# Kernel optimization log

Measured on AMD Instinct MI355X. Metric: run time of the kernel, lower is better.

Reference implementation:

```python
import jax, jax.numpy as jnp
import numpy as np

D = 64      # n_embd (== head_size in this module)
H = 8       # n_heads
B = 4
T = 2048    # seq len == block_size
EPS = 1e-5


def layernorm(x, g, b):
    mu = jnp.mean(x, axis=-1, keepdims=True)
    var = jnp.mean(jnp.square(x - mu), axis=-1, keepdims=True)
    return (x - mu) * jax.lax.rsqrt(var + EPS) * g + b


def setup_inputs() -> dict:
    key = jax.random.key(0)
    ks = jax.random.split(key, 16)
    s = 1.0 / np.sqrt(D)
    inp = {
        'inputs': jax.random.normal(ks[0], (B, T, D), jnp.float32),
        # per-head QKV linears: weight [H, D, D] (in, out), bias [H, D]
        'Wq': jax.random.uniform(ks[1], (H, D, D), jnp.float32, -s, s),
        'bq': jax.random.uniform(ks[2], (H, D), jnp.float32, -s, s),
        'Wk': jax.random.uniform(ks[3], (H, D, D), jnp.float32, -s, s),
        'bk': jax.random.uniform(ks[4], (H, D), jnp.float32, -s, s),
        'Wv': jax.random.uniform(ks[5], (H, D, D), jnp.float32, -s, s),
        'bv': jax.random.uniform(ks[6], (H, D), jnp.float32, -s, s),
        # projection: Linear(H*D -> D)
        'Wp': jax.random.uniform(ks[7], (H * D, D), jnp.float32, -1/np.sqrt(H*D), 1/np.sqrt(H*D)),
        'bp': jax.random.uniform(ks[8], (D,), jnp.float32, -1/np.sqrt(H*D), 1/np.sqrt(H*D)),
        # FFN: D -> 4D -> D
        'W1': jax.random.uniform(ks[9], (D, 4 * D), jnp.float32, -s, s),
        'b1': jax.random.uniform(ks[10], (4 * D,), jnp.float32, -s, s),
        'W2': jax.random.uniform(ks[11], (4 * D, D), jnp.float32, -1/np.sqrt(4*D), 1/np.sqrt(4*D)),
        'b2': jax.random.uniform(ks[12], (D,), jnp.float32, -1/np.sqrt(4*D), 1/np.sqrt(4*D)),
        'g1': jnp.ones((D,), jnp.float32), 'be1': jnp.zeros((D,), jnp.float32),
        'g2': jnp.ones((D,), jnp.float32), 'be2': jnp.zeros((D,), jnp.float32),
    }
    return inp


def reference(inputs, Wq, bq, Wk, bk, Wv, bv, Wp, bp, W1, b1, W2, b2, g1, be1, g2, be2):
    x = inputs
    # per-head full-width QKV: [H, B, T, D]
    q = jnp.einsum('btd,hde->hbte', x, Wq) + bq[:, None, None, :]
    k = jnp.einsum('btd,hde->hbte', x, Wk) + bk[:, None, None, :]
    v = jnp.einsum('btd,hde->hbte', x, Wv) + bv[:, None, None, :]
    # unscaled scores (module has no 1/sqrt(d) scaling)
    scores = jnp.einsum('hbte,hbse->hbts', q, k)  # [H, B, T, T]
    causal = jnp.tril(jnp.ones((T, T), bool))
    scores = jnp.where(causal, scores, -jnp.inf)
    attn = jax.nn.softmax(scores, axis=-1)
    out = jnp.einsum('hbts,hbse->hbte', attn, v)  # [H, B, T, D]
    # torch.cat over heads along last dim -> [B, T, H*D]
    cat = jnp.transpose(out, (1, 2, 0, 3)).reshape(B, T, H * D)
    attn_out = cat @ Wp + bp
    h1 = layernorm(x + attn_out, g1, be1)
    ffn = jax.nn.relu(h1 @ W1 + b1) @ W2 + b2
    return layernorm(h1 + ffn, g2, be2)
```

## Files before the change

kernel.cpp:

```cpp
#include <hip/hip_runtime.h>
#include <hip/hip_bf16.h>
#include <stdint.h>

#define Dd 64
#define Hh 8
#define Bb 4
#define Tt 2048
#define NT (Bb * Tt)

typedef __attribute__((ext_vector_type(4))) float f32x4;
typedef __attribute__((ext_vector_type(8))) __bf16 bf16x8;
typedef __attribute__((ext_vector_type(8))) uint16_t u16x8;
typedef __attribute__((ext_vector_type(4))) uint16_t u16x4;

__device__ __forceinline__ uint16_t f2bf_fast(float f) {
    union { __bf16 h; uint16_t u; } c; c.h = (__bf16)f; return c.u;
}
__device__ __forceinline__ uint32_t pkbf(float a, float b) {
    return (uint32_t)f2bf_fast(a) | ((uint32_t)f2bf_fast(b) << 16);
}

#define SWZ(row, k)   ((row) * 72  + ((k) ^ ((((row) >> 3) & 7) << 3)))
#define PSZ(q, k)     ((q)  * 72  + ((k) ^ ((((q)  >> 2) & 3) << 3)))
#define HSZ(q, k)     ((q)  * 264 + ((k) ^ ((((q)  >> 2) & 3) << 3)))
#define W2SWZ(col, k) ((col) * 264 + ((k) ^ ((((col) >> 3) & 7) << 3)))
#define WPSWZ(col, k) ((col) * 520 + ((k) ^ ((((col) >> 3) & 7) << 3)))

__global__ __launch_bounds__(256) void setup_kernel(
    const float* __restrict__ Wp, const float* __restrict__ W1,
    const float* __restrict__ W2,
    uint16_t* __restrict__ WptS, uint16_t* __restrict__ W1g,
    uint16_t* __restrict__ W2g)
{
    const int bid = blockIdx.x, t = threadIdx.x;
    if (bid < 8) {
        const int j = bid;
#pragma unroll
        for (int p = 0; p < 16; ++p) {
            int idx = p * 256 + t;
            int col = idx & 63, k = j * 64 + (idx >> 6);
            WptS[WPSWZ(col, k)] = f2bf_fast(Wp[(size_t)k * 64 + col]);
        }
    } else if (bid < 12) {
        const int j = bid - 8;
#pragma unroll
        for (int p = 0; p < 16; ++p) {
            int e = j * 4096 + p * 256 + t;
            int col = e & 255, k = e >> 8;
            W1g[SWZ(col, k)] = f2bf_fast(W1[(size_t)k * 256 + col]);
        }
    } else {
        const int j = bid - 12;
#pragma unroll
        for (int p = 0; p < 16; ++p) {
            int e = j * 4096 + p * 256 + t;
            int col = e & 63, k = e >> 6;
            W2g[W2SWZ(col, k)] = f2bf_fast(W2[(size_t)k * 64 + col]);
        }
    }
}

__global__ __launch_bounds__(256) void qkv_kernel(
    const float* __restrict__ x,
    const float* __restrict__ Wq, const float* __restrict__ bq,
    const float* __restrict__ Wk, const float* __restrict__ bk,
    const float* __restrict__ Wv, const float* __restrict__ bv,
    uint16_t* __restrict__ qb, uint16_t* __restrict__ kb, uint16_t* __restrict__ vb)
{
    __shared__ uint16_t WtF[64 * 72];
    const int rt = blockIdx.x, h = blockIdx.y, m = blockIdx.z;
    const float* W    = (m == 0) ? Wq : (m == 1) ? Wk : Wv;
    const float* bias = (m == 0) ? bq : (m == 1) ? bk : bv;
    uint16_t*    out  = (m == 0) ? qb : (m == 1) ? kb : vb;
    const int t = threadIdx.x, lane = t & 63, w = t >> 6;
    const int l15 = lane & 15, g = lane >> 4;

#pragma unroll
    for (int p = 0; p < 4; ++p) {
        int idx = p * 256 + t;
        int r = idx >> 4, c4 = (idx & 15) * 4;
        f32x4 wv = *(const f32x4*)&W[(size_t)(h * 64 + r) * 64 + c4];
#pragma unroll
        for (int j = 0; j < 4; ++j) WtF[SWZ(c4 + j, r)] = f2bf_fast(wv[j]);
    }
    const int row = rt * 64 + w * 16 + l15;
    union { u16x8 u; bf16x8 b; } a0, a1;
    {
        f32x4 x0 = *(const f32x4*)&x[(size_t)row * 64 + g * 8];
        f32x4 x1 = *(const f32x4*)&x[(size_t)row * 64 + g * 8 + 4];
        f32x4 x2 = *(const f32x4*)&x[(size_t)row * 64 + 32 + g * 8];
        f32x4 x3 = *(const f32x4*)&x[(size_t)row * 64 + 32 + g * 8 + 4];
#pragma unroll
        for (int j = 0; j < 4; ++j) {
            a0.u[j] = f2bf_fast(x0[j]); a0.u[4 + j] = f2bf_fast(x1[j]);
            a1.u[j] = f2bf_fast(x2[j]); a1.u[4 + j] = f2bf_fast(x3[j]);
        }
    }
    __syncthreads();

    f32x4 acc[4] = {};
#pragma unroll
    for (int ct = 0; ct < 4; ++ct) {
        bf16x8 b0 = *(const bf16x8*)&WtF[SWZ(ct * 16 + l15, g * 8)];
        bf16x8 b1 = *(const bf16x8*)&WtF[SWZ(ct * 16 + l15, 32 + g * 8)];
        acc[ct] = __builtin_amdgcn_mfma_f32_16x16x32_bf16(a0.b, b0, acc[ct], 0, 0, 0);
        acc[ct] = __builtin_amdgcn_mfma_f32_16x16x32_bf16(a1.b, b1, acc[ct], 0, 0, 0);
    }
#pragma unroll
    for (int ct = 0; ct < 4; ++ct) {
        float bb = bias[h * 64 + ct * 16 + l15];
#pragma unroll
        for (int rr = 0; rr < 4; ++rr) {
            int orow = rt * 64 + w * 16 + g * 4 + rr;
            out[((size_t)h * NT + orow) * 64 + ct * 16 + l15] =
                f2bf_fast(acc[ct][rr] + bb);
        }
    }
}

__global__ __launch_bounds__(128) void attn_kernel5(
    const uint16_t* __restrict__ qb, const uint16_t* __restrict__ kb,
    const uint16_t* __restrict__ vb, uint16_t* __restrict__ cat)
{
    __shared__ uint16_t KsF[2][64 * 72];
    __shared__ uint16_t VtF[2][64 * 72];
    const int bid = blockIdx.x;
    const int lbid = (bid & 7) * 128 + (bid >> 3);
    const int pairid = lbid & 31;
    const int hb = lbid >> 5;
    const int h = hb & 7, b = hb >> 3;
    const int t = threadIdx.x, lane = t & 63, w = t >> 6;
    const int l15 = lane & 15, g = lane >> 4;
    const size_t base = ((size_t)h * NT + (size_t)b * Tt) * 64;
    const uint16_t* Qh = qb + base;
    const uint16_t* Kh = kb + base;
    const uint16_t* Vh = vb + base;

    for (int ph = 0; ph < 2; ++ph) {
        const int qt32 = ph ? (63 - pairid) : pairid;
        bf16x8 aq0, aq1;
        {
            int qrow = qt32 * 32 + w * 16 + l15;
            aq0 = *(const bf16x8*)&Qh[(size_t)qrow * 64 + g * 8];
            aq1 = *(const bf16x8*)&Qh[(size_t)qrow * 64 + 32 + g * 8];
        }
        f32x4 o[4] = {};
        float m_run = -INFINITY, l_run = 0.f;

        __syncthreads();
#pragma unroll
        for (int i = 0; i < 4; ++i) {
            int slot = i * 128 + t;
            int r = slot >> 3, c8 = (slot & 7) * 8;
            u16x8 kk = *(const u16x8*)&Kh[(size_t)r * 64 + c8];
            u16x8 vv = *(const u16x8*)&Vh[(size_t)r * 64 + c8];
            *(u16x8*)&KsF[0][SWZ(r, c8)] = kk;
#pragma unroll
            for (int j = 0; j < 8; ++j) VtF[0][SWZ(c8 + j, r)] = vv[j];
        }
        __syncthreads();

        const int nkv = (qt32 >> 1) + 1;
        for (int kv = 0; kv < nkv; ++kv) {
            const int cur = kv & 1;
            const bool pf = (kv + 1) < nkv;
            u16x8 pK[4], pV[4];
            if (pf) {
#pragma unroll
                for (int i = 0; i < 4; ++i) {
                    int slot = i * 128 + t;
                    int r = (kv + 1) * 64 + (slot >> 3), c8 = (slot & 7) * 8;
                    pK[i] = *(const u16x8*)&Kh[(size_t)r * 64 + c8];
                    pV[i] = *(const u16x8*)&Vh[(size_t)r * 64 + c8];
                }
            }
            f32x4 s[4];
#pragma unroll
            for (int kt = 0; kt < 4; ++kt) {
                bf16x8 bk0 = *(const bf16x8*)&KsF[cur][SWZ(kt * 16 + l15, g * 8)];
                bf16x8 bk1 = *(const bf16x8*)&KsF[cur][SWZ(kt * 16 + l15, 32 + g * 8)];
                f32x4 z = {};
                z = __builtin_amdgcn_mfma_f32_16x16x32_bf16(bk0, aq0, z, 0, 0, 0);
                z = __builtin_amdgcn_mfma_f32_16x16x32_bf16(bk1, aq1, z, 0, 0, 0);
                s[kt] = z;
            }
            if (kv == nkv - 1) {
                int qlocal = (qt32 & 1) * 32 + w * 16 + l15;
#pragma unroll
                for (int kt = 0; kt < 4; ++kt)
#pragma unroll
                    for (int rj = 0; rj < 4; ++rj)
                        if (kt * 16 + g * 4 + rj > qlocal) s[kt][rj] = -INFINITY;
            }
            float mt = s[0][0];
#pragma unroll
            for (int kt = 0; kt < 4; ++kt)
#pragma unroll
                for (int rj = 0; rj < 4; ++rj) mt = fmaxf(mt, s[kt][rj]);
            mt = fmaxf(mt, __shfl_xor(mt, 16));
            mt = fmaxf(mt, __shfl_xor(mt, 32));
            if (__any((int)(mt > m_run + 8.f))) {
                float mnew = fmaxf(m_run, mt);
                float alpha = __expf(m_run - mnew);
                m_run = mnew;
                l_run *= alpha;
                float a0 = __shfl(alpha, g * 4 + 0);
                float a1 = __shfl(alpha, g * 4 + 1);
                float a2 = __shfl(alpha, g * 4 + 2);
                float a3 = __shfl(alpha, g * 4 + 3);
#pragma unroll
                for (int dt = 0; dt < 4; ++dt) {
                    o[dt][0] *= a0; o[dt][1] *= a1; o[dt][2] *= a2; o[dt][3] *= a3;
                }
            }
            float ls = 0.f;
#pragma unroll
            for (int kt = 0; kt < 4; ++kt)
#pragma unroll
                for (int rj = 0; rj < 4; ++rj) {
                    float p = __expf(s[kt][rj] - m_run);
                    s[kt][rj] = p;
                    ls += p;
                }
            ls += __shfl_xor(ls, 16);
            ls += __shfl_xor(ls, 32);
            l_run += ls;
            union { uint32_t wd[4]; bf16x8 v; } ap0, ap1;
            ap0.wd[0] = pkbf(s[0][0], s[0][1]); ap0.wd[1] = pkbf(s[0][2], s[0][3]);
            ap0.wd[2] = pkbf(s[1][0], s[1][1]); ap0.wd[3] = pkbf(s[1][2], s[1][3]);
            ap1.wd[0] = pkbf(s[2][0], s[2][1]); ap1.wd[1] = pkbf(s[2][2], s[2][3]);
            ap1.wd[2] = pkbf(s[3][0], s[3][1]); ap1.wd[3] = pkbf(s[3][2], s[3][3]);
#pragma unroll
            for (int c = 0; c < 2; ++c) {
                const bf16x8 ap = c ? ap1.v : ap0.v;
#pragma unroll
                for (int dt = 0; dt < 4; ++dt) {
                    union { u16x4 q[2]; bf16x8 v; } bb;
                    bb.q[0] = *(const u16x4*)&VtF[cur][SWZ(dt * 16 + l15, c * 32 + g * 4)];
                    bb.q[1] = *(const u16x4*)&VtF[cur][SWZ(dt * 16 + l15, c * 32 + 16 + g * 4)];
                    o[dt] = __builtin_amdgcn_mfma_f32_16x16x32_bf16(ap, bb.v, o[dt], 0, 0, 0);
                }
            }
            if (pf) {
#pragma unroll
                for (int i = 0; i < 4; ++i) {
                    int slot = i * 128 + t;
                    int r = slot >> 3, c8 = (slot & 7) * 8;
                    *(u16x8*)&KsF[cur ^ 1][SWZ(r, c8)] = pK[i];
#pragma unroll
                    for (int j = 0; j < 8; ++j) VtF[cur ^ 1][SWZ(c8 + j, r)] = pV[i][j];
                }
                __syncthreads();
            }
        }
        float inv = 1.f / l_run;
        float i0 = __shfl(inv, g * 4 + 0);
        float i1 = __shfl(inv, g * 4 + 1);
        float i2 = __shfl(inv, g * 4 + 2);
        float i3 = __shfl(inv, g * 4 + 3);
#pragma unroll
        for (int dt = 0; dt < 4; ++dt) {
            int rowb = qt32 * 32 + w * 16 + g * 4;
            size_t cb = ((size_t)b * Tt + rowb) * 512 + h * 64 + dt * 16 + l15;
            cat[cb]         = f2bf_fast(o[dt][0] * i0);
            cat[cb + 512]   = f2bf_fast(o[dt][1] * i1);
            cat[cb + 1024]  = f2bf_fast(o[dt][2] * i2);
            cat[cb + 1536]  = f2bf_fast(o[dt][3] * i3);
        }
    }
}

__global__ __launch_bounds__(128) void tail_kernel(
    const uint16_t* __restrict__ cat, const uint16_t* __restrict__ WptS,
    const uint16_t* __restrict__ W1g, const uint16_t* __restrict__ W2g,
    const float* __restrict__ bp, const float* __restrict__ b1,
    const float* __restrict__ b2, const float* __restrict__ x,
    const float* __restrict__ g1, const float* __restrict__ be1,
    const float* __restrict__ g2, const float* __restrict__ be2,
    float* __restrict__ out)
{
    __shared__ uint16_t h1S[2][16 * 72];
    __shared__ uint16_t hidS[2][16 * 264];
    const int rt = blockIdx.x;
    const int t = threadIdx.x, lane = t & 63, w = t >> 6;
    const int l15 = lane & 15, g = lane >> 4;
    const int arow = rt * 32 + w * 16 + l15;

    f32x4 acc[4] = {};
#pragma unroll
    for (int kt = 0; kt < 16; ++kt) {
        bf16x8 a = *(const bf16x8*)&cat[(size_t)arow * 512 + kt * 32 + g * 8];
#pragma unroll
        for (int ct = 0; ct < 4; ++ct) {
            bf16x8 bfr = *(const bf16x8*)&WptS[WPSWZ(ct * 16 + l15, kt * 32 + g * 8)];
            acc[ct] = __builtin_amdgcn_mfma_f32_16x16x32_bf16(a, bfr, acc[ct], 0, 0, 0);
        }
    }
    float bpv[4], g1v[4], b1v[4];
#pragma unroll
    for (int ct = 0; ct < 4; ++ct) {
        bpv[ct] = bp[ct * 16 + l15];
        g1v[ct] = g1[ct * 16 + l15];
        b1v[ct] = be1[ct * 16 + l15];
    }
    float hv[4][4];
#pragma unroll
    for (int rr = 0; rr < 4; ++rr) {
        int drow = rt * 32 + w * 16 + g * 4 + rr;
        float s[4], sum = 0.f;
#pragma unroll
        for (int ct = 0; ct < 4; ++ct) {
            s[ct] = acc[ct][rr] + bpv[ct] + x[(size_t)drow * 64 + ct * 16 + l15];
            sum += s[ct];
        }
        sum += __shfl_xor(sum, 1); sum += __shfl_xor(sum, 2);
        sum += __shfl_xor(sum, 4); sum += __shfl_xor(sum, 8);
        float mu = sum * (1.f / 64.f);
        float v = 0.f;
#pragma unroll
        for (int ct = 0; ct < 4; ++ct) { s[ct] -= mu; v += s[ct] * s[ct]; }
        v += __shfl_xor(v, 1); v += __shfl_xor(v, 2);
        v += __shfl_xor(v, 4); v += __shfl_xor(v, 8);
        float rstd = rsqrtf(v * (1.f / 64.f) + 1e-5f);
#pragma unroll
        for (int ct = 0; ct < 4; ++ct) {
            float h = s[ct] * rstd * g1v[ct] + b1v[ct];
            hv[ct][rr] = h;
            h1S[w][PSZ(g * 4 + rr, ct * 16 + l15)] = f2bf_fast(h);
        }
    }
    bf16x8 ha0 = *(const bf16x8*)&h1S[w][PSZ(l15, g * 8)];
    bf16x8 ha1 = *(const bf16x8*)&h1S[w][PSZ(l15, 32 + g * 8)];
#pragma unroll
    for (int nt = 0; nt < 16; ++nt) {
        f32x4 a1c = {};
        bf16x8 w10 = *(const bf16x8*)&W1g[SWZ(nt * 16 + l15, g * 8)];
        bf16x8 w11 = *(const bf16x8*)&W1g[SWZ(nt * 16 + l15, 32 + g * 8)];
        a1c = __builtin_amdgcn_mfma_f32_16x16x32_bf16(ha0, w10, a1c, 0, 0, 0);
        a1c = __builtin_amdgcn_mfma_f32_16x16x32_bf16(ha1, w11, a1c, 0, 0, 0);
        float bb1 = b1[nt * 16 + l15];
#pragma unroll
        for (int rr = 0; rr < 4; ++rr)
            hidS[w][HSZ(g * 4 + rr, nt * 16 + l15)] =
                f2bf_fast(fmaxf(a1c[rr] + bb1, 0.f));
    }
    f32x4 acc2[4] = {};
#pragma unroll
    for (int ks = 0; ks < 8; ++ks) {
        bf16x8 hfr = *(const bf16x8*)&hidS[w][HSZ(l15, ks * 32 + g * 8)];
#pragma unroll
        for (int ct = 0; ct < 4; ++ct) {
            bf16x8 w2f = *(const bf16x8*)&W2g[W2SWZ(ct * 16 + l15, ks * 32 + g * 8)];
            acc2[ct] = __builtin_amdgcn_mfma_f32_16x16x32_bf16(hfr, w2f, acc2[ct], 0, 0, 0);
        }
    }
    float b2v[4], g2v[4], be2v[4];
#pragma unroll
    for (int ct = 0; ct < 4; ++ct) {
        b2v[ct]  = b2[ct * 16 + l15];
        g2v[ct]  = g2[ct * 16 + l15];
        be2v[ct] = be2[ct * 16 + l15];
    }
#pragma unroll
    for (int rr = 0; rr < 4; ++rr) {
        int drow = rt * 32 + w * 16 + g * 4 + rr;
        float s[4], sum = 0.f;
#pragma unroll
        for (int ct = 0; ct < 4; ++ct) {
            s[ct] = acc2[ct][rr] + b2v[ct] + hv[ct][rr];
            sum += s[ct];
        }
        sum += __shfl_xor(sum, 1); sum += __shfl_xor(sum, 2);
        sum += __shfl_xor(sum, 4); sum += __shfl_xor(sum, 8);
        float mu = sum * (1.f / 64.f);
        float v = 0.f;
#pragma unroll
        for (int ct = 0; ct < 4; ++ct) { s[ct] -= mu; v += s[ct] * s[ct]; }
        v += __shfl_xor(v, 1); v += __shfl_xor(v, 2);
        v += __shfl_xor(v, 4); v += __shfl_xor(v, 8);
        float rstd = rsqrtf(v * (1.f / 64.f) + 1e-5f);
#pragma unroll
        for (int ct = 0; ct < 4; ++ct)
            out[(size_t)drow * 64 + ct * 16 + l15] =
                s[ct] * rstd * g2v[ct] + be2v[ct];
    }
}

extern "C" void kernel_launch(void* const* d_in, const int* in_sizes, int n_in,
                              void* d_out, int out_size, void* d_ws, size_t ws_size,
                              hipStream_t stream)
{
    (void)in_sizes; (void)n_in; (void)out_size; (void)ws_size;
    const float* x   = (const float*)d_in[0];
    const float* Wq  = (const float*)d_in[1];
    const float* bq  = (const float*)d_in[2];
    const float* Wk  = (const float*)d_in[3];
    const float* bk  = (const float*)d_in[4];
    const float* Wv  = (const float*)d_in[5];
    const float* bv  = (const float*)d_in[6];
    const float* Wp  = (const float*)d_in[7];
    const float* bp  = (const float*)d_in[8];
    const float* W1  = (const float*)d_in[9];
    const float* b1  = (const float*)d_in[10];
    const float* W2  = (const float*)d_in[11];
    const float* b2  = (const float*)d_in[12];
    const float* g1  = (const float*)d_in[13];
    const float* be1 = (const float*)d_in[14];
    const float* g2  = (const float*)d_in[15];
    const float* be2 = (const float*)d_in[16];
    float* outp = (float*)d_out;

    char* w = (char*)d_ws;
    uint16_t* qb   = (uint16_t*)w;
    uint16_t* kb   = qb + (size_t)Hh * NT * 64;
    uint16_t* vb   = kb + (size_t)Hh * NT * 64;
    uint16_t* cat  = vb + (size_t)Hh * NT * 64;
    uint16_t* WptS = cat + (size_t)NT * 512;
    uint16_t* W1g  = WptS + 33280;
    uint16_t* W2g  = W1g + 18432;

    setup_kernel<<<dim3(16), dim3(256), 0, stream>>>(Wp, W1, W2, WptS, W1g, W2g);
    qkv_kernel<<<dim3(NT / 64, Hh, 3), dim3(256), 0, stream>>>(
        x, Wq, bq, Wk, bk, Wv, bv, qb, kb, vb);
    attn_kernel5<<<dim3(1024), dim3(128), 0, stream>>>(qb, kb, vb, cat);
    tail_kernel<<<dim3(256), dim3(128), 0, stream>>>(
        cat, WptS, W1g, W2g, bp, b1, b2, x, g1, be1, g2, be2, outp);
}
```

Baseline: 175.2 us.

## Store V pre-transposed per tile and pre-convert x and QKV weights to bf16

The QKV kernel now writes V transposed within each 64-row tile, so the attention kernel can copy V into shared memory with vectorized 16-byte stores. This replaces the eight scalar transposing shared-memory writes per chunk in the inner KV loop. The setup kernel also converts x and the per-head Wq/Wk/Wv to bf16 (weights pre-swizzled) once, so the 1536 QKV blocks no longer convert x and the weights redundantly. The cost is extra workspace, an extra pass over x, and strided 8-byte V stores in the QKV kernel.

```diff
diff --git a/kernel.cpp b/kernel.cpp
--- a/kernel.cpp
+++ b/kernel.cpp
@@ -27,22 +27,45 @@
 #define WPSWZ(col, k) ((col) * 520 + ((k) ^ ((((col) >> 3) & 7) << 3)))
 
 __global__ __launch_bounds__(256) void setup_kernel(
-    const float* __restrict__ Wp, const float* __restrict__ W1,
-    const float* __restrict__ W2,
+    const float* __restrict__ x,
+    const float* __restrict__ Wq, const float* __restrict__ Wk,
+    const float* __restrict__ Wv, const float* __restrict__ Wp,
+    const float* __restrict__ W1, const float* __restrict__ W2,
+    uint16_t* __restrict__ xb, uint16_t* __restrict__ WtAll,
     uint16_t* __restrict__ WptS, uint16_t* __restrict__ W1g,
     uint16_t* __restrict__ W2g)
 {
     const int bid = blockIdx.x, t = threadIdx.x;
-    if (bid < 8) {
-        const int j = bid;
+    if (bid < 256) {
+        size_t base = ((size_t)bid * 256 + t) * 8;
+        f32x4 a = *(const f32x4*)&x[base];
+        f32x4 b = *(const f32x4*)&x[base + 4];
+        u16x8 o;
+#pragma unroll
+        for (int j = 0; j < 4; ++j) { o[j] = f2bf_fast(a[j]); o[4 + j] = f2bf_fast(b[j]); }
+        *(u16x8*)&xb[base] = o;
+    } else if (bid < 280) {
+        const int mh = bid - 256, m = mh / 8, h = mh % 8;
+        const float* W = (m == 0) ? Wq : (m == 1) ? Wk : Wv;
+        uint16_t* dst = WtAll + (size_t)mh * 4608;
+#pragma unroll
+        for (int p = 0; p < 4; ++p) {
+            int idx = p * 256 + t;
+            int k = idx >> 4, c4 = (idx & 15) * 4;
+            f32x4 wv = *(const f32x4*)&W[(size_t)(h * 64 + k) * 64 + c4];
+#pragma unroll
+            for (int j = 0; j < 4; ++j) dst[SWZ(c4 + j, k)] = f2bf_fast(wv[j]);
+        }
+    } else if (bid < 288) {
+        const int j = bid - 280;
 #pragma unroll
         for (int p = 0; p < 16; ++p) {
             int idx = p * 256 + t;
             int col = idx & 63, k = j * 64 + (idx >> 6);
             WptS[WPSWZ(col, k)] = f2bf_fast(Wp[(size_t)k * 64 + col]);
         }
-    } else if (bid < 12) {
-        const int j = bid - 8;
+    } else if (bid < 292) {
+        const int j = bid - 288;
 #pragma unroll
         for (int p = 0; p < 16; ++p) {
             int e = j * 4096 + p * 256 + t;
@@ -50,7 +73,7 @@
             W1g[SWZ(col, k)] = f2bf_fast(W1[(size_t)k * 256 + col]);
         }
     } else {
-        const int j = bid - 12;
+        const int j = bid - 292;
 #pragma unroll
         for (int p = 0; p < 16; ++p) {
             int e = j * 4096 + p * 256 + t;
@@ -61,41 +84,27 @@
 }
 
 __global__ __launch_bounds__(256) void qkv_kernel(
-    const float* __restrict__ x,
-    const float* __restrict__ Wq, const float* __restrict__ bq,
-    const float* __restrict__ Wk, const float* __restrict__ bk,
-    const float* __restrict__ Wv, const float* __restrict__ bv,
+    const uint16_t* __restrict__ xb, const uint16_t* __restrict__ WtAll,
+    const float* __restrict__ bq, const float* __restrict__ bk,
+    const float* __restrict__ bv,
     uint16_t* __restrict__ qb, uint16_t* __restrict__ kb, uint16_t* __restrict__ vb)
 {
     __shared__ uint16_t WtF[64 * 72];
     const int rt = blockIdx.x, h = blockIdx.y, m = blockIdx.z;
-    const float* W    = (m == 0) ? Wq : (m == 1) ? Wk : Wv;
     const float* bias = (m == 0) ? bq : (m == 1) ? bk : bv;
-    uint16_t*    out  = (m == 0) ? qb : (m == 1) ? kb : vb;
     const int t = threadIdx.x, lane = t & 63, w = t >> 6;
     const int l15 = lane & 15, g = lane >> 4;
 
-#pragma unroll
-    for (int p = 0; p < 4; ++p) {
-        int idx = p * 256 + t;
-        int r = idx >> 4, c4 = (idx & 15) * 4;
-        f32x4 wv = *(const f32x4*)&W[(size_t)(h * 64 + r) * 64 + c4];
-#pragma unroll
-        for (int j = 0; j < 4; ++j) WtF[SWZ(c4 + j, r)] = f2bf_fast(wv[j]);
+    {
+        const u16x8* src = (const u16x8*)(WtAll + (size_t)(m * 8 + h) * 4608);
+        u16x8* dst = (u16x8*)WtF;
+        dst[t] = src[t];
+        dst[256 + t] = src[256 + t];
+        if (t < 64) dst[512 + t] = src[512 + t];
     }
     const int row = rt * 64 + w * 16 + l15;
-    union { u16x8 u; bf16x8 b; } a0, a1;
-    {
-        f32x4 x0 = *(const f32x4*)&x[(size_t)row * 64 + g * 8];
-        f32x4 x1 = *(const f32x4*)&x[(size_t)row * 64 + g * 8 + 4];
-        f32x4 x2 = *(const f32x4*)&x[(size_t)row * 64 + 32 + g * 8];
-        f32x4 x3 = *(const f32x4*)&x[(size_t)row * 64 + 32 + g * 8 + 4];
-#pragma unroll
-        for (int j = 0; j < 4; ++j) {
-            a0.u[j] = f2bf_fast(x0[j]); a0.u[4 + j] = f2bf_fast(x1[j]);
-            a1.u[j] = f2bf_fast(x2[j]); a1.u[4 + j] = f2bf_fast(x3[j]);
-        }
-    }
+    bf16x8 a0 = *(const bf16x8*)&xb[(size_t)row * 64 + g * 8];
+    bf16x8 a1 = *(const bf16x8*)&xb[(size_t)row * 64 + 32 + g * 8];
     __syncthreads();
 
     f32x4 acc[4] = {};
@@ -103,22 +112,35 @@
     for (int ct = 0; ct < 4; ++ct) {
         bf16x8 b0 = *(const bf16x8*)&WtF[SWZ(ct * 16 + l15, g * 8)];
         bf16x8 b1 = *(const bf16x8*)&WtF[SWZ(ct * 16 + l15, 32 + g * 8)];
-        acc[ct] = __builtin_amdgcn_mfma_f32_16x16x32_bf16(a0.b, b0, acc[ct], 0, 0, 0);
-        acc[ct] = __builtin_amdgcn_mfma_f32_16x16x32_bf16(a1.b, b1, acc[ct], 0, 0, 0);
-    }
-#pragma unroll
-    for (int ct = 0; ct < 4; ++ct) {
-        float bb = bias[h * 64 + ct * 16 + l15];
-#pragma unroll
-        for (int rr = 0; rr < 4; ++rr) {
-            int orow = rt * 64 + w * 16 + g * 4 + rr;
-            out[((size_t)h * NT + orow) * 64 + ct * 16 + l15] =
-                f2bf_fast(acc[ct][rr] + bb);
-        }
-    }
-}
-
-__global__ __launch_bounds__(128) void attn_kernel5(
+        acc[ct] = __builtin_amdgcn_mfma_f32_16x16x32_bf16(a0, b0, acc[ct], 0, 0, 0);
+        acc[ct] = __builtin_amdgcn_mfma_f32_16x16x32_bf16(a1, b1, acc[ct], 0, 0, 0);
+    }
+    if (m < 2) {
+        uint16_t* out = (m == 0) ? qb : kb;
+#pragma unroll
+        for (int ct = 0; ct < 4; ++ct) {
+            float bb = bias[h * 64 + ct * 16 + l15];
+#pragma unroll
+            for (int rr = 0; rr < 4; ++rr) {
+                int orow = rt * 64 + w * 16 + g * 4 + rr;
+                out[((size_t)h * NT + orow) * 64 + ct * 16 + l15] =
+                    f2bf_fast(acc[ct][rr] + bb);
+            }
+        }
+    } else {
+        const size_t tb = ((size_t)h * NT + (size_t)rt * 64) * 64;
+#pragma unroll
+        for (int ct = 0; ct < 4; ++ct) {
+            float bb = bias[h * 64 + ct * 16 + l15];
+            u16x4 vo;
+#pragma unroll
+            for (int rr = 0; rr < 4; ++rr) vo[rr] = f2bf_fast(acc[ct][rr] + bb);
+            *(u16x4*)&vb[tb + (size_t)(ct * 16 + l15) * 64 + w * 16 + g * 4] = vo;
+        }
+    }
+}
+
+__global__ __launch_bounds__(128) void attn_kernel6(
     const uint16_t* __restrict__ qb, const uint16_t* __restrict__ kb,
     const uint16_t* __restrict__ vb, uint16_t* __restrict__ cat)
 {
@@ -132,9 +154,9 @@
     const int t = threadIdx.x, lane = t & 63, w = t >> 6;
     const int l15 = lane & 15, g = lane >> 4;
     const size_t base = ((size_t)h * NT + (size_t)b * Tt) * 64;
-    const uint16_t* Qh = qb + base;
-    const uint16_t* Kh = kb + base;
-    const uint16_t* Vh = vb + base;
+    const uint16_t* Qh  = qb + base;
+    const uint16_t* Kh  = kb + base;
+    const uint16_t* VhT = vb + base;
 
     for (int ph = 0; ph < 2; ++ph) {
         const int qt32 = ph ? (63 - pairid) : pairid;
@@ -152,11 +174,11 @@
         for (int i = 0; i < 4; ++i) {
             int slot = i * 128 + t;
             int r = slot >> 3, c8 = (slot & 7) * 8;
-            u16x8 kk = *(const u16x8*)&Kh[(size_t)r * 64 + c8];
-            u16x8 vv = *(const u16x8*)&Vh[(size_t)r * 64 + c8];
+            size_t off = (size_t)r * 64 + c8;
+            u16x8 kk = *(const u16x8*)&Kh[off];
+            u16x8 vv = *(const u16x8*)&VhT[off];
             *(u16x8*)&KsF[0][SWZ(r, c8)] = kk;
-#pragma unroll
-            for (int j = 0; j < 8; ++j) VtF[0][SWZ(c8 + j, r)] = vv[j];
+            *(u16x8*)&VtF[0][SWZ(r, c8)] = vv;
         }
         __syncthreads();
 
@@ -166,12 +188,13 @@
             const bool pf = (kv + 1) < nkv;
             u16x8 pK[4], pV[4];
             if (pf) {
+                const size_t poff = (size_t)(kv + 1) * 4096;
 #pragma unroll
                 for (int i = 0; i < 4; ++i) {
                     int slot = i * 128 + t;
-                    int r = (kv + 1) * 64 + (slot >> 3), c8 = (slot & 7) * 8;
-                    pK[i] = *(const u16x8*)&Kh[(size_t)r * 64 + c8];
-                    pV[i] = *(const u16x8*)&Vh[(size_t)r * 64 + c8];
+                    size_t off = poff + (size_t)(slot >> 3) * 64 + (slot & 7) * 8;
+                    pK[i] = *(const u16x8*)&Kh[off];
+                    pV[i] = *(const u16x8*)&VhT[off];
                 }
             }
             f32x4 s[4];
@@ -247,8 +270,7 @@
                     int slot = i * 128 + t;
                     int r = slot >> 3, c8 = (slot & 7) * 8;
                     *(u16x8*)&KsF[cur ^ 1][SWZ(r, c8)] = pK[i];
-#pragma unroll
-                    for (int j = 0; j < 8; ++j) VtF[cur ^ 1][SWZ(c8 + j, r)] = pV[i][j];
+                    *(u16x8*)&VtF[cur ^ 1][SWZ(r, c8)] = pV[i];
                 }
                 __syncthreads();
             }
@@ -262,10 +284,10 @@
         for (int dt = 0; dt < 4; ++dt) {
             int rowb = qt32 * 32 + w * 16 + g * 4;
             size_t cb = ((size_t)b * Tt + rowb) * 512 + h * 64 + dt * 16 + l15;
-            cat[cb]         = f2bf_fast(o[dt][0] * i0);
-            cat[cb + 512]   = f2bf_fast(o[dt][1] * i1);
-            cat[cb + 1024]  = f2bf_fast(o[dt][2] * i2);
-            cat[cb + 1536]  = f2bf_fast(o[dt][3] * i3);
+            cat[cb]        = f2bf_fast(o[dt][0] * i0);
+            cat[cb + 512]  = f2bf_fast(o[dt][1] * i1);
+            cat[cb + 1024] = f2bf_fast(o[dt][2] * i2);
+            cat[cb + 1536] = f2bf_fast(o[dt][3] * i3);
         }
     }
 }
@@ -418,11 +440,14 @@
     uint16_t* WptS = cat + (size_t)NT * 512;
     uint16_t* W1g  = WptS + 33280;
     uint16_t* W2g  = W1g + 18432;
-
-    setup_kernel<<<dim3(16), dim3(256), 0, stream>>>(Wp, W1, W2, WptS, W1g, W2g);
+    uint16_t* xb   = W2g + 16896;
+    uint16_t* WtAll= xb + (size_t)NT * 64;
+
+    setup_kernel<<<dim3(296), dim3(256), 0, stream>>>(
+        x, Wq, Wk, Wv, Wp, W1, W2, xb, WtAll, WptS, W1g, W2g);
     qkv_kernel<<<dim3(NT / 64, Hh, 3), dim3(256), 0, stream>>>(
-        x, Wq, bq, Wk, bk, Wv, bv, qb, kb, vb);
-    attn_kernel5<<<dim3(1024), dim3(128), 0, stream>>>(qb, kb, vb, cat);
+        xb, WtAll, bq, bk, bv, qb, kb, vb);
+    attn_kernel6<<<dim3(1024), dim3(128), 0, stream>>>(qb, kb, vb, cat);
     tail_kernel<<<dim3(256), dim3(128), 0, stream>>>(
         cat, WptS, W1g, W2g, bp, b1, b2, x, g1, be1, g2, be2, outp);
 }
```

After: 167.9 us. -4.2%, faster.
